# Kernel optimization log

Measured on AMD Instinct MI355X. Metric: run time of the kernel, lower is better.

The kernel has to match this reference:

```python
import jax, jax.numpy as jnp
import numpy as np
import math

B = 32768
INPUT_SIZE = 256
PROJ_DIM = 64


def setup_inputs() -> dict:
    key = jax.random.key(0)
    ks = jax.random.split(key, 9)
    def lin(kw, kb, fan_in, fan_out):
        bound = 1.0 / math.sqrt(fan_in)
        W = jax.random.uniform(kw, (fan_out, fan_in), jnp.float32, -bound, bound)
        b = jax.random.uniform(kb, (fan_out,), jnp.float32, -bound, bound)
        return W, b
    Wq, bq = lin(ks[0], ks[1], INPUT_SIZE, PROJ_DIM)
    Wk, bk = lin(ks[2], ks[3], INPUT_SIZE, PROJ_DIM)
    Wv, bv = lin(ks[4], ks[5], INPUT_SIZE, PROJ_DIM)
    Wo, bo = lin(ks[6], ks[7], PROJ_DIM, INPUT_SIZE)
    x = jax.random.normal(ks[8], (B, INPUT_SIZE), jnp.float32)
    return {"x": x, "Wq": Wq, "bq": bq, "Wk": Wk, "bk": bk,
            "Wv": Wv, "bv": bv, "Wo": Wo, "bo": bo}


def reference(x, Wq, bq, Wk, bk, Wv, bv, Wo, bo):
    scale = math.sqrt(PROJ_DIM)
    q = x @ Wq.T + bq  # [B, P]
    k = x @ Wk.T + bk  # [B, P]
    v = x @ Wv.T + bv  # [B, P]
    # per-sample outer product: scores[b, i, j] = q[b, i] * k[b, j] / scale
    scores = (q[:, :, None] * k[:, None, :]) / scale  # [B, P, P]
    attn = jax.nn.softmax(scores, axis=-1)
    out = jnp.einsum("bij,bj->bi", attn, v)  # [B, P]
    return out @ Wo.T + bo  # [B, input_size]
```

## Files before the change

### kernel.cpp

```cpp
#include <hip/hip_runtime.h>
#include <hip/hip_bf16.h>
#include <stdint.h>

typedef __attribute__((ext_vector_type(4))) float f32x4;
typedef __attribute__((ext_vector_type(8))) short s16x8;

#define KSCALE 0.1803368801111204f

__device__ __forceinline__ short f2bf(float x) {
  __bf16 h = (__bf16)x;
  return __builtin_bit_cast(short, h);
}

__global__ void prep_kernel(const float* __restrict__ Wq, const float* __restrict__ Wk,
                            const float* __restrict__ Wv, const float* __restrict__ bq,
                            const float* __restrict__ bk, const float* __restrict__ bv,
                            const float* __restrict__ Wo,
                            short* __restrict__ wqkv, short* __restrict__ wo,
                            float* __restrict__ bias) {
  int idx = blockIdx.x * 256 + threadIdx.x;
  if (idx < 192 * 256) {
    int r = idx >> 8, c = idx & 255;
    float v;
    if (r < 64)       v = Wq[r * 256 + c];
    else if (r < 128) v = Wk[(r - 64) * 256 + c] * KSCALE;
    else              v = Wv[(r - 128) * 256 + c];
    wqkv[idx] = f2bf(v);
  } else if (idx < 192 * 256 + 256 * 64) {
    int i2 = idx - 192 * 256;
    wo[i2] = f2bf(Wo[i2]);
  } else if (idx < 192 * 256 + 256 * 64 + 192) {
    int r = idx - (192 * 256 + 256 * 64);
    float v = (r < 64) ? bq[r] : (r < 128) ? bk[r - 64] * KSCALE : bv[r - 128];
    bias[r] = v;
  }
}

__global__ __launch_bounds__(256, 8)
void fused_attn(const float* __restrict__ x,
                const short* __restrict__ wqkv,
                const short* __restrict__ wo,
                const float* __restrict__ biasqkv,
                const float* __restrict__ bo,
                float* __restrict__ out) {
  __shared__ __align__(16) char smem[14336];
  const int tid = threadIdx.x;
  const int lane = tid & 63;
  const int w = tid >> 6;
  const int l15 = lane & 15;
  const int g = lane >> 4;
  const int rowbase = blockIdx.x * 16;

#pragma unroll
  for (int it = 0; it < 4; ++it) {
    int flat4 = it * 256 + tid;
    int r = flat4 >> 6;
    int c4 = flat4 & 63;
    const f32x4 xv = *reinterpret_cast<const f32x4*>(x + (size_t)(rowbase + r) * 256 + c4 * 4);
    unsigned p0 = (unsigned short)f2bf(xv[0]) | ((unsigned)(unsigned short)f2bf(xv[1]) << 16);
    unsigned p1 = (unsigned short)f2bf(xv[2]) | ((unsigned)(unsigned short)f2bf(xv[3]) << 16);
    int byte = (r * 512 + c4 * 8) ^ ((r & 7) << 4);
    uint2* p = reinterpret_cast<uint2*>(smem + byte);
    p->x = p0; p->y = p1;
  }
  __syncthreads();

  f32x4 acc1[3];
#pragma unroll
  for (int ct = 0; ct < 3; ++ct) acc1[ct] = (f32x4){0.f, 0.f, 0.f, 0.f};

  const int ct0 = w * 3;
#pragma unroll
  for (int ks = 0; ks < 8; ++ks) {
    int byteA = (l15 * 512 + ks * 64 + g * 16) ^ ((l15 & 7) << 4);
    s16x8 afr = *reinterpret_cast<const s16x8*>(smem + byteA);
#pragma unroll
    for (int ct = 0; ct < 3; ++ct) {
      int n = (ct0 + ct) * 16 + l15;
      s16x8 bfr = *reinterpret_cast<const s16x8*>(wqkv + (size_t)n * 256 + ks * 32 + g * 8);
      acc1[ct] = __builtin_amdgcn_mfma_f32_16x16x32_bf16(afr, bfr, acc1[ct], 0, 0, 0);
    }
  }
  __syncthreads();

#pragma unroll
  for (int ct = 0; ct < 3; ++ct) {
    int cg = (ct0 + ct) * 16 + l15;
    float bb = biasqkv[cg];
    int arr = cg >> 6;
    int cc = cg & 63;
    int base = arr * 4096;
#pragma unroll
    for (int rg = 0; rg < 4; ++rg) {
      int r = g * 4 + rg;
      int byte = (base + r * 256 + cc * 4) ^ ((r & 7) << 4);
      *reinterpret_cast<float*>(smem + byte) = acc1[ct][rg] + bb;
    }
  }
  __syncthreads();

#pragma unroll 1
  for (int si = 0; si < 4; ++si) {
    int s = w * 4 + si;
    int swz = (s & 7) << 4;
    f32x4 kf[2][2];
#pragma unroll
    for (int jh = 0; jh < 2; ++jh) {
      int raw = 4096 + s * 256 + jh * 128 + g * 32;
      kf[jh][0] = *reinterpret_cast<const f32x4*>(smem + (raw ^ swz));
      kf[jh][1] = *reinterpret_cast<const f32x4*>(smem + ((raw + 16) ^ swz));
    }
    s16x8 vfr[2];
#pragma unroll
    for (int jh = 0; jh < 2; ++jh) {
      s16x8 t = (s16x8){0, 0, 0, 0, 0, 0, 0, 0};
      if (l15 == 0) {
        int raw = 8192 + s * 256 + jh * 128 + g * 32;
        f32x4 v0 = *reinterpret_cast<const f32x4*>(smem + (raw ^ swz));
        f32x4 v1 = *reinterpret_cast<const f32x4*>(smem + ((raw + 16) ^ swz));
        t[0] = f2bf(v0[0]); t[1] = f2bf(v0[1]); t[2] = f2bf(v0[2]); t[3] = f2bf(v0[3]);
        t[4] = f2bf(v1[0]); t[5] = f2bf(v1[1]); t[6] = f2bf(v1[2]); t[7] = f2bf(v1[3]);
      } else if (l15 == 1) {
        short one = f2bf(1.0f);
        t = (s16x8){one, one, one, one, one, one, one, one};
      }
      vfr[jh] = t;
    }
#pragma unroll
    for (int it = 0; it < 4; ++it) {
      int rawq = s * 256 + (it * 16 + l15) * 4;
      float qi = *reinterpret_cast<const float*>(smem + (rawq ^ swz));
      f32x4 acc = (f32x4){0.f, 0.f, 0.f, 0.f};
#pragma unroll
      for (int jh = 0; jh < 2; ++jh) {
        s16x8 ef;
#pragma unroll
        for (int h = 0; h < 2; ++h)
#pragma unroll
          for (int e4 = 0; e4 < 4; ++e4)
            ef[h * 4 + e4] = f2bf(__builtin_amdgcn_exp2f(qi * kf[jh][h][e4]));
        acc = __builtin_amdgcn_mfma_f32_16x16x32_bf16(vfr[jh], ef, acc, 0, 0, 0);
      }
      if (lane < 16) {
        float o = acc[0] * __builtin_amdgcn_rcpf(acc[1]);
        int raw = 12288 + s * 128 + (it * 16 + lane) * 2;
        *reinterpret_cast<short*>(smem + (raw ^ swz)) = f2bf(o);
      }
    }
  }
  __syncthreads();

  f32x4 acc3[4];
#pragma unroll
  for (int ct = 0; ct < 4; ++ct) acc3[ct] = (f32x4){0.f, 0.f, 0.f, 0.f};
  const int ct3 = w * 4;
#pragma unroll
  for (int ks = 0; ks < 2; ++ks) {
    int byteA = (12288 + l15 * 128 + ks * 64 + g * 16) ^ ((l15 & 7) << 4);
    s16x8 afr = *reinterpret_cast<const s16x8*>(smem + byteA);
#pragma unroll
    for (int ct = 0; ct < 4; ++ct) {
      int n = (ct3 + ct) * 16 + l15;
      s16x8 bfr = *reinterpret_cast<const s16x8*>(wo + (size_t)n * 64 + ks * 32 + g * 8);
      acc3[ct] = __builtin_amdgcn_mfma_f32_16x16x32_bf16(afr, bfr, acc3[ct], 0, 0, 0);
    }
  }
#pragma unroll
  for (int ct = 0; ct < 4; ++ct) {
    int n = (ct3 + ct) * 16 + l15;
    float bov = bo[n];
#pragma unroll
    for (int rg = 0; rg < 4; ++rg) {
      int r = rowbase + g * 4 + rg;
      out[(size_t)r * 256 + n] = acc3[ct][rg] + bov;
    }
  }
}

extern "C" void kernel_launch(void* const* d_in, const int* in_sizes, int n_in,
                              void* d_out, int out_size, void* d_ws, size_t ws_size,
                              hipStream_t stream) {
  const float* x  = (const float*)d_in[0];
  const float* Wq = (const float*)d_in[1];
  const float* bq = (const float*)d_in[2];
  const float* Wk = (const float*)d_in[3];
  const float* bk = (const float*)d_in[4];
  const float* Wv = (const float*)d_in[5];
  const float* bv = (const float*)d_in[6];
  const float* Wo = (const float*)d_in[7];
  const float* bo = (const float*)d_in[8];
  float* out = (float*)d_out;

  short* wqkv = (short*)d_ws;
  short* wo   = wqkv + 192 * 256;
  float* bias = (float*)((char*)d_ws + 131072);

  prep_kernel<<<257, 256, 0, stream>>>(Wq, Wk, Wv, bq, bk, bv, Wo, wqkv, wo, bias);
  fused_attn<<<2048, 256, 0, stream>>>(x, wqkv, wo, bias, bo, out);
}
```

Measured before the change: 132.0 us.

## Software-pipeline per-sample attention loads and drop a barrier via separate LDS regions

Q/K/V are now written to a separate LDS region after the x tile, so the barrier between the first GEMM and the bias store is no longer needed. The per-sample attention loop is fully unrolled with double-buffered register sets, loading the next sample's K, V and q while computing the current one. V is loaded by all lanes and selected branch-free instead of in a divergent branch. LDS grows from 14 KB to 22 KB and launch bounds drop from 8 to 4 blocks per SM, so register pressure and occupancy trade against the added latency hiding.

```diff
diff --git a/kernel.cpp b/kernel.cpp
--- a/kernel.cpp
+++ b/kernel.cpp
@@ -36,14 +36,78 @@
   }
 }
 
-__global__ __launch_bounds__(256, 8)
+struct SReg {
+  f32x4 kf[2][2];
+  f32x4 vv[2][2];
+  float q[4];
+};
+
+__device__ __forceinline__ void load_sample(const char* __restrict__ smem, int s,
+                                            int g, int l15, SReg& R) {
+  const int swz = (s & 7) << 4;
+#pragma unroll
+  for (int jh = 0; jh < 2; ++jh) {
+    int rawk = 12288 + s * 256 + jh * 128 + g * 32;
+    R.kf[jh][0] = *reinterpret_cast<const f32x4*>(smem + (rawk ^ swz));
+    R.kf[jh][1] = *reinterpret_cast<const f32x4*>(smem + ((rawk + 16) ^ swz));
+    int rawv = 16384 + s * 256 + jh * 128 + g * 32;
+    R.vv[jh][0] = *reinterpret_cast<const f32x4*>(smem + (rawv ^ swz));
+    R.vv[jh][1] = *reinterpret_cast<const f32x4*>(smem + ((rawv + 16) ^ swz));
+  }
+#pragma unroll
+  for (int it = 0; it < 4; ++it) {
+    int rawq = 8192 + s * 256 + (it * 16 + l15) * 4;
+    R.q[it] = *reinterpret_cast<const float*>(smem + (rawq ^ swz));
+  }
+}
+
+__device__ __forceinline__ void compute_sample(char* __restrict__ smem, int s,
+                                               int g, int l15, int lane, const SReg& R) {
+  const int swz = (s & 7) << 4;
+  const short one = f2bf(1.0f);
+  s16x8 vfr[2];
+#pragma unroll
+  for (int jh = 0; jh < 2; ++jh) {
+    s16x8 t;
+#pragma unroll
+    for (int h = 0; h < 2; ++h)
+#pragma unroll
+      for (int e = 0; e < 4; ++e) {
+        short vb = f2bf(R.vv[jh][h][e]);
+        t[h * 4 + e] = (l15 == 0) ? vb : ((l15 == 1) ? one : (short)0);
+      }
+    vfr[jh] = t;
+  }
+#pragma unroll
+  for (int it = 0; it < 4; ++it) {
+    float qi = R.q[it];
+    f32x4 acc = (f32x4){0.f, 0.f, 0.f, 0.f};
+#pragma unroll
+    for (int jh = 0; jh < 2; ++jh) {
+      s16x8 ef;
+#pragma unroll
+      for (int h = 0; h < 2; ++h)
+#pragma unroll
+        for (int e = 0; e < 4; ++e)
+          ef[h * 4 + e] = f2bf(__builtin_amdgcn_exp2f(qi * R.kf[jh][h][e]));
+      acc = __builtin_amdgcn_mfma_f32_16x16x32_bf16(vfr[jh], ef, acc, 0, 0, 0);
+    }
+    if (lane < 16) {
+      float o = acc[0] * __builtin_amdgcn_rcpf(acc[1]);
+      int raw = 20480 + s * 128 + (it * 16 + lane) * 2;
+      *reinterpret_cast<short*>(smem + (raw ^ swz)) = f2bf(o);
+    }
+  }
+}
+
+__global__ __launch_bounds__(256, 4)
 void fused_attn(const float* __restrict__ x,
                 const short* __restrict__ wqkv,
                 const short* __restrict__ wo,
                 const float* __restrict__ biasqkv,
                 const float* __restrict__ bo,
                 float* __restrict__ out) {
-  __shared__ __align__(16) char smem[14336];
+  __shared__ __align__(16) char smem[22528];
   const int tid = threadIdx.x;
   const int lane = tid & 63;
   const int w = tid >> 6;
@@ -81,7 +145,6 @@
       acc1[ct] = __builtin_amdgcn_mfma_f32_16x16x32_bf16(afr, bfr, acc1[ct], 0, 0, 0);
     }
   }
-  __syncthreads();
 
 #pragma unroll
   for (int ct = 0; ct < 3; ++ct) {
@@ -89,7 +152,7 @@
     float bb = biasqkv[cg];
     int arr = cg >> 6;
     int cc = cg & 63;
-    int base = arr * 4096;
+    int base = 8192 + arr * 4096;
 #pragma unroll
     for (int rg = 0; rg < 4; ++rg) {
       int r = g * 4 + rg;
@@ -99,54 +162,17 @@
   }
   __syncthreads();
 
-#pragma unroll 1
-  for (int si = 0; si < 4; ++si) {
-    int s = w * 4 + si;
-    int swz = (s & 7) << 4;
-    f32x4 kf[2][2];
-#pragma unroll
-    for (int jh = 0; jh < 2; ++jh) {
-      int raw = 4096 + s * 256 + jh * 128 + g * 32;
-      kf[jh][0] = *reinterpret_cast<const f32x4*>(smem + (raw ^ swz));
-      kf[jh][1] = *reinterpret_cast<const f32x4*>(smem + ((raw + 16) ^ swz));
-    }
-    s16x8 vfr[2];
-#pragma unroll
-    for (int jh = 0; jh < 2; ++jh) {
-      s16x8 t = (s16x8){0, 0, 0, 0, 0, 0, 0, 0};
-      if (l15 == 0) {
-        int raw = 8192 + s * 256 + jh * 128 + g * 32;
-        f32x4 v0 = *reinterpret_cast<const f32x4*>(smem + (raw ^ swz));
-        f32x4 v1 = *reinterpret_cast<const f32x4*>(smem + ((raw + 16) ^ swz));
-        t[0] = f2bf(v0[0]); t[1] = f2bf(v0[1]); t[2] = f2bf(v0[2]); t[3] = f2bf(v0[3]);
-        t[4] = f2bf(v1[0]); t[5] = f2bf(v1[1]); t[6] = f2bf(v1[2]); t[7] = f2bf(v1[3]);
-      } else if (l15 == 1) {
-        short one = f2bf(1.0f);
-        t = (s16x8){one, one, one, one, one, one, one, one};
-      }
-      vfr[jh] = t;
-    }
-#pragma unroll
-    for (int it = 0; it < 4; ++it) {
-      int rawq = s * 256 + (it * 16 + l15) * 4;
-      float qi = *reinterpret_cast<const float*>(smem + (rawq ^ swz));
-      f32x4 acc = (f32x4){0.f, 0.f, 0.f, 0.f};
-#pragma unroll
-      for (int jh = 0; jh < 2; ++jh) {
-        s16x8 ef;
-#pragma unroll
-        for (int h = 0; h < 2; ++h)
-#pragma unroll
-          for (int e4 = 0; e4 < 4; ++e4)
-            ef[h * 4 + e4] = f2bf(__builtin_amdgcn_exp2f(qi * kf[jh][h][e4]));
-        acc = __builtin_amdgcn_mfma_f32_16x16x32_bf16(vfr[jh], ef, acc, 0, 0, 0);
-      }
-      if (lane < 16) {
-        float o = acc[0] * __builtin_amdgcn_rcpf(acc[1]);
-        int raw = 12288 + s * 128 + (it * 16 + lane) * 2;
-        *reinterpret_cast<short*>(smem + (raw ^ swz)) = f2bf(o);
-      }
-    }
+  {
+    const int s0 = w * 4;
+    SReg A, B;
+    load_sample(smem, s0 + 0, g, l15, A);
+    load_sample(smem, s0 + 1, g, l15, B);
+    compute_sample(smem, s0 + 0, g, l15, lane, A);
+    load_sample(smem, s0 + 2, g, l15, A);
+    compute_sample(smem, s0 + 1, g, l15, lane, B);
+    load_sample(smem, s0 + 3, g, l15, B);
+    compute_sample(smem, s0 + 2, g, l15, lane, A);
+    compute_sample(smem, s0 + 3, g, l15, lane, B);
   }
   __syncthreads();
 
@@ -156,7 +182,7 @@
   const int ct3 = w * 4;
 #pragma unroll
   for (int ks = 0; ks < 2; ++ks) {
-    int byteA = (12288 + l15 * 128 + ks * 64 + g * 16) ^ ((l15 & 7) << 4);
+    int byteA = (20480 + l15 * 128 + ks * 64 + g * 16) ^ ((l15 & 7) << 4);
     s16x8 afr = *reinterpret_cast<const s16x8*>(smem + byteA);
 #pragma unroll
     for (int ct = 0; ct < 4; ++ct) {
```

After: 129.0 us. 1.02x faster.

## Split fused attention kernel into QKV projection and scalar-softmax output kernels

Applied to the files above, without the earlier changes.

Splits the single fused kernel into two launches. The first computes Q/K/V projections and writes Q (bf16) and K, V (fp32) to workspace. The second computes the per-sample softmax-weighted sum with scalar exp/FMA per lane instead of the MFMA-based path with a ones-row denominator trick, then applies the output projection. This avoids the wasted MFMA lanes and the bf16 rounding of exp values, but adds an extra kernel launch and a global round trip of roughly 20 MB of intermediates.

```diff
diff --git a/kernel.cpp b/kernel.cpp
--- a/kernel.cpp
+++ b/kernel.cpp
@@ -10,6 +10,10 @@
 __device__ __forceinline__ short f2bf(float x) {
   __bf16 h = (__bf16)x;
   return __builtin_bit_cast(short, h);
+}
+__device__ __forceinline__ float bf2f(unsigned short u) {
+  unsigned x = ((unsigned)u) << 16;
+  return __builtin_bit_cast(float, x);
 }
 
 __global__ void prep_kernel(const float* __restrict__ Wq, const float* __restrict__ Wk,
@@ -36,14 +40,14 @@
   }
 }
 
-__global__ __launch_bounds__(256, 8)
-void fused_attn(const float* __restrict__ x,
-                const short* __restrict__ wqkv,
-                const short* __restrict__ wo,
-                const float* __restrict__ biasqkv,
-                const float* __restrict__ bo,
-                float* __restrict__ out) {
-  __shared__ __align__(16) char smem[14336];
+__global__ __launch_bounds__(256, 4)
+void attn_qkv(const float* __restrict__ x,
+              const short* __restrict__ wqkv,
+              const float* __restrict__ biasqkv,
+              unsigned short* __restrict__ qb,
+              float* __restrict__ kb,
+              float* __restrict__ vb) {
+  __shared__ __align__(16) char smem[22528];
   const int tid = threadIdx.x;
   const int lane = tid & 63;
   const int w = tid >> 6;
@@ -68,7 +72,6 @@
   f32x4 acc1[3];
 #pragma unroll
   for (int ct = 0; ct < 3; ++ct) acc1[ct] = (f32x4){0.f, 0.f, 0.f, 0.f};
-
   const int ct0 = w * 3;
 #pragma unroll
   for (int ks = 0; ks < 8; ++ks) {
@@ -81,7 +84,6 @@
       acc1[ct] = __builtin_amdgcn_mfma_f32_16x16x32_bf16(afr, bfr, acc1[ct], 0, 0, 0);
     }
   }
-  __syncthreads();
 
 #pragma unroll
   for (int ct = 0; ct < 3; ++ct) {
@@ -89,7 +91,7 @@
     float bb = biasqkv[cg];
     int arr = cg >> 6;
     int cc = cg & 63;
-    int base = arr * 4096;
+    int base = 8192 + arr * 4096;
 #pragma unroll
     for (int rg = 0; rg < 4; ++rg) {
       int r = g * 4 + rg;
@@ -99,64 +101,75 @@
   }
   __syncthreads();
 
+  {
+    int row = tid >> 4, c4 = tid & 15;
+    int byq = (8192 + row * 256 + c4 * 16) ^ ((row & 7) << 4);
+    f32x4 qv = *reinterpret_cast<const f32x4*>(smem + byq);
+    uint2 qp;
+    qp.x = (unsigned short)f2bf(qv[0]) | ((unsigned)(unsigned short)f2bf(qv[1]) << 16);
+    qp.y = (unsigned short)f2bf(qv[2]) | ((unsigned)(unsigned short)f2bf(qv[3]) << 16);
+    *reinterpret_cast<uint2*>(qb + (size_t)(rowbase + row) * 64 + c4 * 4) = qp;
+
+    int byk = (12288 + row * 256 + c4 * 16) ^ ((row & 7) << 4);
+    *reinterpret_cast<f32x4*>(kb + (size_t)(rowbase + row) * 64 + c4 * 4) =
+        *reinterpret_cast<const f32x4*>(smem + byk);
+
+    int byv = (16384 + row * 256 + c4 * 16) ^ ((row & 7) << 4);
+    *reinterpret_cast<f32x4*>(vb + (size_t)(rowbase + row) * 64 + c4 * 4) =
+        *reinterpret_cast<const f32x4*>(smem + byv);
+  }
+}
+
+__global__ __launch_bounds__(256, 4)
+void attn_out(const unsigned short* __restrict__ qb,
+              const float* __restrict__ kb,
+              const float* __restrict__ vb,
+              const short* __restrict__ wo,
+              const float* __restrict__ bo,
+              float* __restrict__ out) {
+  __shared__ __align__(16) char smem[2048];
+  const int tid = threadIdx.x;
+  const int lane = tid & 63;
+  const int wu = __builtin_amdgcn_readfirstlane(tid >> 6);
+  const int l15 = lane & 15;
+  const int g = lane >> 4;
+  const int sbase = blockIdx.x * 16;
+
 #pragma unroll 1
   for (int si = 0; si < 4; ++si) {
-    int s = w * 4 + si;
-    int swz = (s & 7) << 4;
-    f32x4 kf[2][2];
-#pragma unroll
-    for (int jh = 0; jh < 2; ++jh) {
-      int raw = 4096 + s * 256 + jh * 128 + g * 32;
-      kf[jh][0] = *reinterpret_cast<const f32x4*>(smem + (raw ^ swz));
-      kf[jh][1] = *reinterpret_cast<const f32x4*>(smem + ((raw + 16) ^ swz));
-    }
-    s16x8 vfr[2];
-#pragma unroll
-    for (int jh = 0; jh < 2; ++jh) {
-      s16x8 t = (s16x8){0, 0, 0, 0, 0, 0, 0, 0};
-      if (l15 == 0) {
-        int raw = 8192 + s * 256 + jh * 128 + g * 32;
-        f32x4 v0 = *reinterpret_cast<const f32x4*>(smem + (raw ^ swz));
-        f32x4 v1 = *reinterpret_cast<const f32x4*>(smem + ((raw + 16) ^ swz));
-        t[0] = f2bf(v0[0]); t[1] = f2bf(v0[1]); t[2] = f2bf(v0[2]); t[3] = f2bf(v0[3]);
-        t[4] = f2bf(v1[0]); t[5] = f2bf(v1[1]); t[6] = f2bf(v1[2]); t[7] = f2bf(v1[3]);
-      } else if (l15 == 1) {
-        short one = f2bf(1.0f);
-        t = (s16x8){one, one, one, one, one, one, one, one};
-      }
-      vfr[jh] = t;
-    }
-#pragma unroll
-    for (int it = 0; it < 4; ++it) {
-      int rawq = s * 256 + (it * 16 + l15) * 4;
-      float qi = *reinterpret_cast<const float*>(smem + (rawq ^ swz));
-      f32x4 acc = (f32x4){0.f, 0.f, 0.f, 0.f};
-#pragma unroll
-      for (int jh = 0; jh < 2; ++jh) {
-        s16x8 ef;
-#pragma unroll
-        for (int h = 0; h < 2; ++h)
-#pragma unroll
-          for (int e4 = 0; e4 < 4; ++e4)
-            ef[h * 4 + e4] = f2bf(__builtin_amdgcn_exp2f(qi * kf[jh][h][e4]));
-        acc = __builtin_amdgcn_mfma_f32_16x16x32_bf16(vfr[jh], ef, acc, 0, 0, 0);
-      }
-      if (lane < 16) {
-        float o = acc[0] * __builtin_amdgcn_rcpf(acc[1]);
-        int raw = 12288 + s * 128 + (it * 16 + lane) * 2;
-        *reinterpret_cast<short*>(smem + (raw ^ swz)) = f2bf(o);
-      }
-    }
+    const int srow = wu * 4 + si;
+    const int s = sbase + srow;
+    const float* kr = kb + (size_t)s * 64;
+    const float* vr = vb + (size_t)s * 64;
+    float qi = bf2f(qb[(size_t)s * 64 + lane]);
+    float num0 = 0.f, num1 = 0.f, num2 = 0.f, num3 = 0.f;
+    float den0 = 0.f, den1 = 0.f, den2 = 0.f, den3 = 0.f;
+#pragma unroll
+    for (int j = 0; j < 64; j += 4) {
+      float e0 = __builtin_amdgcn_exp2f(qi * kr[j + 0]);
+      float e1 = __builtin_amdgcn_exp2f(qi * kr[j + 1]);
+      float e2 = __builtin_amdgcn_exp2f(qi * kr[j + 2]);
+      float e3 = __builtin_amdgcn_exp2f(qi * kr[j + 3]);
+      num0 += e0 * vr[j + 0]; den0 += e0;
+      num1 += e1 * vr[j + 1]; den1 += e1;
+      num2 += e2 * vr[j + 2]; den2 += e2;
+      num3 += e3 * vr[j + 3]; den3 += e3;
+    }
+    float num = (num0 + num1) + (num2 + num3);
+    float den = (den0 + den1) + (den2 + den3);
+    float o = num * __builtin_amdgcn_rcpf(den);
+    int byte = (srow * 128 + lane * 2) ^ ((srow & 7) << 4);
+    *reinterpret_cast<short*>(smem + byte) = f2bf(o);
   }
   __syncthreads();
 
   f32x4 acc3[4];
 #pragma unroll
   for (int ct = 0; ct < 4; ++ct) acc3[ct] = (f32x4){0.f, 0.f, 0.f, 0.f};
-  const int ct3 = w * 4;
+  const int ct3 = wu * 4;
 #pragma unroll
   for (int ks = 0; ks < 2; ++ks) {
-    int byteA = (12288 + l15 * 128 + ks * 64 + g * 16) ^ ((l15 & 7) << 4);
+    int byteA = (l15 * 128 + ks * 64 + g * 16) ^ ((l15 & 7) << 4);
     s16x8 afr = *reinterpret_cast<const s16x8*>(smem + byteA);
 #pragma unroll
     for (int ct = 0; ct < 4; ++ct) {
@@ -171,7 +184,7 @@
     float bov = bo[n];
 #pragma unroll
     for (int rg = 0; rg < 4; ++rg) {
-      int r = rowbase + g * 4 + rg;
+      int r = sbase + g * 4 + rg;
       out[(size_t)r * 256 + n] = acc3[ct][rg] + bov;
     }
   }
@@ -191,10 +204,15 @@
   const float* bo = (const float*)d_in[8];
   float* out = (float*)d_out;
 
-  short* wqkv = (short*)d_ws;
-  short* wo   = wqkv + 192 * 256;
-  float* bias = (float*)((char*)d_ws + 131072);
+  char* ws = (char*)d_ws;
+  short* wqkv = (short*)ws;
+  short* wo   = (short*)(ws + 98304);
+  float* bias = (float*)(ws + 131072);
+  unsigned short* qb = (unsigned short*)(ws + 262144);
+  float* kb = (float*)(ws + 4456448);
+  float* vb = (float*)(ws + 12845056);
 
   prep_kernel<<<257, 256, 0, stream>>>(Wq, Wk, Wv, bq, bk, bv, Wo, wqkv, wo, bias);
-  fused_attn<<<2048, 256, 0, stream>>>(x, wqkv, wo, bias, bo, out);
-}
+  attn_qkv<<<2048, 256, 0, stream>>>(x, wqkv, bias, qb, kb, vb);
+  attn_out<<<2048, 256, 0, stream>>>(qb, kb, vb, wo, bo, out);
+}
```

After: 143.2 us. +8.4%, slower.
